# Performance work log

Hardware: AMD Instinct MI355X
Metric: run time of the kernel (lower is better)

## Reference

```python
import jax, jax.numpy as jnp
import numpy as np


def _lstm(x, Wk, Wr, b, reverse, return_seq):
    # Keras LSTM with activation='relu', recurrent_activation='sigmoid'.
    # Wk: (F, 4H), Wr: (H, 4H), b: (4H). Gate order: i, f, c, o.
    if reverse:
        x = jnp.flip(x, 1)
    H = Wr.shape[0]
    xg = jnp.einsum('btf,fg->btg', x, Wk) + b  # (B, T, 4H)
    B = x.shape[0]

    def step(carry, g_t):
        h, c = carry
        g = g_t + h @ Wr
        i = jax.nn.sigmoid(g[:, :H])
        f = jax.nn.sigmoid(g[:, H:2 * H])
        cc = jax.nn.relu(g[:, 2 * H:3 * H])
        o = jax.nn.sigmoid(g[:, 3 * H:])
        c = f * c + i * cc
        h = o * jax.nn.relu(c)
        return (h, c), h

    init = (jnp.zeros((B, H), x.dtype), jnp.zeros((B, H), x.dtype))
    (h, _), hs = jax.lax.scan(step, init, jnp.swapaxes(xg, 0, 1))
    if return_seq:
        hs = jnp.swapaxes(hs, 0, 1)  # (B, T, H)
        if reverse:
            hs = jnp.flip(hs, 1)
        return hs
    return h


def setup_inputs() -> dict:
    key = jax.random.key(0)
    ks = jax.random.split(key, 24)
    B, LA, T, F = 256, 200, 512, 128
    s = 0.05
    d = {
        'inputA': jax.random.randint(ks[0], (B, LA), 0, 1000),
        'inputB': jax.random.normal(ks[1], (B, T, F), jnp.float32),
        'emb': jax.random.normal(ks[2], (1000, 3), jnp.float32) * s,
        'w1': jax.random.normal(ks[3], (600, 256), jnp.float32) * s,
        'b1': jnp.zeros((256,), jnp.float32),
        'w2': jax.random.normal(ks[4], (256, 128), jnp.float32) * s,
        'b2': jnp.zeros((128,), jnp.float32),
        'w3': jax.random.normal(ks[5], (128, 64), jnp.float32) * s,
        'b3': jnp.zeros((64,), jnp.float32),
        'k1f': jax.random.normal(ks[6], (128, 512), jnp.float32) * s,
        'r1f': jax.random.normal(ks[7], (128, 512), jnp.float32) * s,
        'bb1f': jnp.zeros((512,), jnp.float32),
        'k1b': jax.random.normal(ks[8], (128, 512), jnp.float32) * s,
        'r1b': jax.random.normal(ks[9], (128, 512), jnp.float32) * s,
        'bb1b': jnp.zeros((512,), jnp.float32),
        'k2f': jax.random.normal(ks[10], (256, 256), jnp.float32) * s,
        'r2f': jax.random.normal(ks[11], (64, 256), jnp.float32) * s,
        'bb2f': jnp.zeros((256,), jnp.float32),
        'k2b': jax.random.normal(ks[12], (256, 256), jnp.float32) * s,
        'r2b': jax.random.normal(ks[13], (64, 256), jnp.float32) * s,
        'bb2b': jnp.zeros((256,), jnp.float32),
        'wz1': jax.random.normal(ks[14], (192, 2), jnp.float32) * s,
        'bz1': jnp.zeros((2,), jnp.float32),
        'wz2': jax.random.normal(ks[15], (2, 1), jnp.float32) * s,
        'bz2': jnp.zeros((1,), jnp.float32),
        'wt1': jax.random.normal(ks[16], (192, 2), jnp.float32) * s,
        'bt1': jnp.zeros((2,), jnp.float32),
        'wt2': jax.random.normal(ks[17], (2, 1), jnp.float32) * s,
        'bt2': jnp.zeros((1,), jnp.float32),
    }
    return d


def reference(inputA, inputB, emb, w1, b1, w2, b2, w3, b3,
              k1f, r1f, bb1f, k1b, r1b, bb1b,
              k2f, r2f, bb2f, k2b, r2b, bb2b,
              wz1, bz1, wz2, bz2, wt1, bt1, wt2, bt2):
    B = inputA.shape[0]
    # Embedding branch
    x = emb[inputA]                       # (B, LA, 3)
    x = x.reshape(B, -1)                  # flatten -> (B, 600)
    x = jax.nn.relu(x @ w1 + b1)
    x = jax.nn.relu(x @ w2 + b2)
    x = jax.nn.relu(x @ w3 + b3)          # (B, 64)
    # BiLSTM branch
    y_f = _lstm(inputB, k1f, r1f, bb1f, reverse=False, return_seq=True)
    y_b = _lstm(inputB, k1b, r1b, bb1b, reverse=True, return_seq=True)
    y = jnp.concatenate([y_f, y_b], axis=-1)   # (B, T, 256)
    h_f = _lstm(y, k2f, r2f, bb2f, reverse=False, return_seq=False)
    h_b = _lstm(y, k2b, r2b, bb2b, reverse=True, return_seq=False)
    y = jnp.concatenate([h_f, h_b], axis=-1)    # (B, 128)
    combined = jnp.concatenate([x, y], axis=-1)  # (B, 192)
    z = jax.nn.relu(combined @ wz1 + bz1) @ wz2 + bz2
    t = jax.nn.relu(combined @ wt1 + bt1) @ wt2 + bt2
    return (z, t)
```

## Files before the change

### kernel.cpp

```cpp
#include <hip/hip_runtime.h>

typedef __attribute__((ext_vector_type(8))) short s8v;
typedef __attribute__((ext_vector_type(4))) short s4v;
typedef __attribute__((ext_vector_type(4))) float f4v;

#if __has_builtin(__builtin_amdgcn_exp2f)
#define EXP2(x) __builtin_amdgcn_exp2f(x)
#else
#define EXP2(x) exp2f(x)
#endif
#if __has_builtin(__builtin_amdgcn_rcpf)
#define RCP(x) __builtin_amdgcn_rcpf(x)
#else
#define RCP(x) (1.0f/(x))
#endif

#define LOG2E 1.4426950408889634f

__device__ __forceinline__ short f2bf(float f) {
    union { float f; unsigned u; } x; x.f = f;
    unsigned r = (x.u + 0x7FFFu + ((x.u >> 16) & 1u)) >> 16;
    return (short)r;
}
__device__ __forceinline__ float bf2f(short s) {
    union { unsigned u; float f; } x; x.u = ((unsigned)(unsigned short)s) << 16;
    return x.f;
}
__device__ __forceinline__ void lds_barrier() {
    asm volatile("s_waitcnt lgkmcnt(0)\n\ts_barrier" ::: "memory");
}

__global__ __launch_bounds__(256) void prep_embed_kernel(
        const float* __restrict__ k1f, const float* __restrict__ r1f,
        const float* __restrict__ k1b, const float* __restrict__ r1b,
        const float* __restrict__ k2f, const float* __restrict__ r2f,
        const float* __restrict__ k2b, const float* __restrict__ r2b,
        short* __restrict__ WB1, short* __restrict__ WB2,
        const int* __restrict__ inputA, const float* __restrict__ emb,
        const float* __restrict__ w1, const float* __restrict__ b1,
        const float* __restrict__ w2, const float* __restrict__ b2,
        const float* __restrict__ w3, const float* __restrict__ b3,
        float* __restrict__ xe) {
    if (blockIdx.x < 1024) {
        int idx = blockIdx.x * 256 + threadIdx.x;
        if (idx < 262144) {
            int j = idx & 7, l = (idx >> 3) & 63, c = (idx >> 9) & 7, n = (idx >> 12) & 31, d = (idx >> 17) & 1;
            int coln = n * 16 + (l & 15);
            int k = c * 32 + ((l >> 4) * 8) + j;
            const float* Wk = d ? k1b : k1f;
            const float* Wr = d ? r1b : r1f;
            float v = (c < 4) ? Wk[k * 512 + coln] : Wr[(k - 128) * 512 + coln];
            float sc = ((n >> 3) == 2) ? 1.0f : -LOG2E;
            WB1[idx] = f2bf(v * sc);
        }
        if (idx < 163840) {
            int d = idx / 81920, r0 = idx % 81920;
            int n = r0 / 5120, r1 = r0 % 5120;
            int c = r1 / 512, li = r1 % 512;
            int l = li >> 3, j = li & 7;
            int coln = n * 16 + (l & 15);
            int k = c * 32 + ((l >> 4) * 8) + j;
            const float* Wk = d ? k2b : k2f;
            const float* Wr = d ? r2b : r2f;
            float v = (k < 256) ? Wk[k * 256 + coln] : Wr[(k - 256) * 256 + coln];
            float sc = ((n >> 2) == 2) ? 1.0f : -LOG2E;
            WB2[idx] = f2bf(v * sc);
        }
        return;
    }
    __shared__ float row[600];
    __shared__ float h1[256];
    __shared__ float h2[128];
    int b = blockIdx.x - 1024, t = threadIdx.x;
    if (t < 200) {
        int idx = inputA[b * 200 + t];
        row[t * 3 + 0] = emb[idx * 3 + 0];
        row[t * 3 + 1] = emb[idx * 3 + 1];
        row[t * 3 + 2] = emb[idx * 3 + 2];
    }
    __syncthreads();
    float a = b1[t];
    for (int k = 0; k < 600; k++) a += row[k] * w1[k * 256 + t];
    h1[t] = fmaxf(a, 0.f);
    __syncthreads();
    if (t < 128) {
        float a2 = b2[t];
        for (int k = 0; k < 256; k++) a2 += h1[k] * w2[k * 128 + t];
        h2[t] = fmaxf(a2, 0.f);
    }
    __syncthreads();
    if (t < 64) {
        float a3 = b3[t];
        for (int k = 0; k < 128; k++) a3 += h2[k] * w3[k * 64 + t];
        xe[b * 64 + t] = fmaxf(a3, 0.f);
    }
}

__global__ __launch_bounds__(512, 2) void megastep(
        const float* __restrict__ x, const short* __restrict__ WB1, const short* __restrict__ WB2,
        const float* __restrict__ bb1f, const float* __restrict__ bb1b,
        const float* __restrict__ bb2f, const float* __restrict__ bb2b,
        short* __restrict__ yfr, short* __restrict__ xgA, short* __restrict__ xgB,
        short* __restrict__ ygA, short* __restrict__ ygB,
        float* __restrict__ c1st, short* __restrict__ h1st,
        float* __restrict__ c2st, short* __restrict__ h2st,
        float* __restrict__ h2o, int k, int TC, int NC) {
    __shared__ short hA[2048];
    __shared__ short hB[2048];
    __shared__ short stg[38912];
    const int tid = threadIdx.x, lane = tid & 63, w = tid >> 6;
    const int bid = blockIdx.x;
    const int tgn = TC >> 3;

    if (bid < 32) {
        const int cl = k - 1;
        if (cl < 0 || cl >= NC) return;
        const int t0 = cl * TC;
        const int first = (cl == 0);
        const int btile = bid & 15, dir = bid >> 4;
        const int col = lane & 15, q = lane >> 4, u = (w << 4) + col;
        const int sb = dir * 16 + btile;

        s8v wf[4][4];
#pragma unroll
        for (int ti = 0; ti < 4; ti++)
#pragma unroll
            for (int c = 0; c < 4; c++)
                wf[ti][c] = *(const s8v*)(WB1 + ((((dir * 32 + (w + 8 * ti)) * 8) + 4 + c) * 64 + lane) * 8);

        float cst[4], hl[4];
        if (first) {
#pragma unroll
            for (int r = 0; r < 4; r++) cst[r] = 0.f;
            for (int i = tid; i < 2048; i += 512) hA[i] = 0;
        } else {
            f4v cv = *(const f4v*)(c1st + ((size_t)sb * 8 + w) * 256 + lane * 4);
#pragma unroll
            for (int r = 0; r < 4; r++) cst[r] = cv[r];
            for (int i = tid; i < 2048; i += 512) hA[i] = h1st[sb * 2048 + i];
        }
        __syncthreads();

        const short* xgp = ((cl & 1) ? xgB : xgA) + (size_t)sb * TC * 8192 + w * 1024 + lane * 8;
        s8v pe0 = *(const s8v*)(xgp);
        s8v pe1 = *(const s8v*)(xgp + 512);
        s8v po0 = *(const s8v*)(xgp + 8192);
        s8v po1 = *(const s8v*)(xgp + 8192 + 512);

        const int hidx = (w >> 1) * 512 + ((u >> 3) & 3) * 128 + (u & 7);

        for (int s = 0; s < TC; s += 2) {
            {
                s8v ah[4];
#pragma unroll
                for (int cc = 0; cc < 4; cc++) ah[cc] = *(const s8v*)&hA[(cc * 64 + lane) * 8];
                if (w >= 4 && s > 0) {
                    int tp = t0 + s - 1;
                    if (dir) tp = 511 - tp;
                    s8v hv = (w == 4) ? ah[0] : (w == 5) ? ah[1] : (w == 6) ? ah[2] : ah[3];
                    *(s8v*)(yfr + (((size_t)(btile * 512 + tp) * 8) + dir * 4 + (w - 4)) * 512 + lane * 8) = hv;
                }
                f4v acc[4];
#pragma unroll
                for (int r = 0; r < 4; r++) {
                    acc[0][r] = bf2f(pe0[r]);
                    acc[1][r] = bf2f(pe0[4 + r]);
                    acc[2][r] = bf2f(pe1[r]);
                    acc[3][r] = bf2f(pe1[4 + r]);
                }
                {
                    const short* np = xgp + (size_t)(s + 2) * 8192;
                    pe0 = *(const s8v*)np;
                    pe1 = *(const s8v*)(np + 512);
                }
#pragma unroll
                for (int cc = 0; cc < 4; cc++)
#pragma unroll
                    for (int ti = 0; ti < 4; ti++)
                        acc[ti] = __builtin_amdgcn_mfma_f32_16x16x32_bf16(ah[cc], wf[ti][cc], acc[ti], 0, 0, 0);
#pragma unroll
                for (int r = 0; r < 4; r++) {
                    float iv = RCP(1.0f + EXP2(acc[0][r]));
                    float fv = RCP(1.0f + EXP2(acc[1][r]));
                    float ov = RCP(1.0f + EXP2(acc[3][r]));
                    float ccv = fmaxf(acc[2][r], 0.f);
                    cst[r] = fv * cst[r] + iv * ccv;
                    hl[r] = ov * fmaxf(cst[r], 0.f);
                }
#pragma unroll
                for (int r = 0; r < 4; r++)
                    hB[hidx + ((q * 4 + r) << 3)] = f2bf(hl[r]);
                lds_barrier();
            }
            {
                s8v ah[4];
#pragma unroll
                for (int cc = 0; cc < 4; cc++) ah[cc] = *(const s8v*)&hB[(cc * 64 + lane) * 8];
                if (w >= 4) {
                    int tp = t0 + s;
                    if (dir) tp = 511 - tp;
                    s8v hv = (w == 4) ? ah[0] : (w == 5) ? ah[1] : (w == 6) ? ah[2] : ah[3];
                    *(s8v*)(yfr + (((size_t)(btile * 512 + tp) * 8) + dir * 4 + (w - 4)) * 512 + lane * 8) = hv;
                }
                f4v acc[4];
#pragma unroll
                for (int r = 0; r < 4; r++) {
                    acc[0][r] = bf2f(po0[r]);
                    acc[1][r] = bf2f(po0[4 + r]);
                    acc[2][r] = bf2f(po1[r]);
                    acc[3][r] = bf2f(po1[4 + r]);
                }
                {
                    const short* np = xgp + (size_t)(s + 3) * 8192;
                    po0 = *(const s8v*)np;
                    po1 = *(const s8v*)(np + 512);
                }
#pragma unroll
                for (int cc = 0; cc < 4; cc++)
#pragma unroll
                    for (int ti = 0; ti < 4; ti++)
                        acc[ti] = __builtin_amdgcn_mfma_f32_16x16x32_bf16(ah[cc], wf[ti][cc], acc[ti], 0, 0, 0);
#pragma unroll
                for (int r = 0; r < 4; r++) {
                    float iv = RCP(1.0f + EXP2(acc[0][r]));
                    float fv = RCP(1.0f + EXP2(acc[1][r]));
                    float ov = RCP(1.0f + EXP2(acc[3][r]));
                    float ccv = fmaxf(acc[2][r], 0.f);
                    cst[r] = fv * cst[r] + iv * ccv;
                    hl[r] = ov * fmaxf(cst[r], 0.f);
                }
#pragma unroll
                for (int r = 0; r < 4; r++)
                    hA[hidx + ((q * 4 + r) << 3)] = f2bf(hl[r]);
                lds_barrier();
            }
        }
        if (w >= 4) {
            int tp = t0 + TC - 1;
            if (dir) tp = 511 - tp;
            s8v hv = *(const s8v*)&hA[((w - 4) * 64 + lane) * 8];
            *(s8v*)(yfr + (((size_t)(btile * 512 + tp) * 8) + dir * 4 + (w - 4)) * 512 + lane * 8) = hv;
        }
        f4v cv;
#pragma unroll
        for (int r = 0; r < 4; r++) cv[r] = cst[r];
        *(f4v*)(c1st + ((size_t)sb * 8 + w) * 256 + lane * 4) = cv;
        for (int i = tid; i < 2048; i += 512) h1st[sb * 2048 + i] = hA[i];
        return;
    }

    if (bid < 64) {
        const int c2 = k - 3;
        if (c2 < 0 || c2 >= NC) return;
        const int first = (c2 == 0), last = (c2 == NC - 1);
        const int btile = (bid - 32) & 15, dir = (bid - 32) >> 4;
        const int b0 = btile << 4;
        const int w4 = w & 3;
        const int col = lane & 15, q = lane >> 4, u = (w4 << 4) + col;
        const int sb = dir * 16 + btile;

        s8v wf[4][2];
#pragma unroll
        for (int ti = 0; ti < 4; ti++)
#pragma unroll
            for (int c = 0; c < 2; c++)
                wf[ti][c] = *(const s8v*)(WB2 + ((((dir * 16 + (w4 + 4 * ti)) * 10) + 8 + c) * 64 + lane) * 8);

        float cst[4], hl[4] = {0.f, 0.f, 0.f, 0.f};
        if (first) {
#pragma unroll
            for (int r = 0; r < 4; r++) cst[r] = 0.f;
            for (int i = tid; i < 1024; i += 512) hA[i] = 0;
        } else {
            f4v cv = *(const f4v*)(c2st + ((size_t)sb * 4 + w4) * 256 + lane * 4);
#pragma unroll
            for (int r = 0; r < 4; r++) cst[r] = cv[r];
            for (int i = tid; i < 1024; i += 512) hA[i] = h2st[sb * 1024 + i];
        }
        __syncthreads();

        const short* ygp = ((c2 & 1) ? ygB : ygA) + (size_t)sb * TC * 4096 + w4 * 1024 + lane * 8;
        s8v pe0, pe1, po0, po1;
        if (w < 4) {
            pe0 = *(const s8v*)(ygp);
            pe1 = *(const s8v*)(ygp + 512);
            po0 = *(const s8v*)(ygp + 4096);
            po1 = *(const s8v*)(ygp + 4096 + 512);
        }
        const int hidx = (w4 >> 1) * 512 + ((u >> 3) & 3) * 128 + (u & 7);

        for (int s = 0; s < TC; s += 2) {
            if (w < 4) {
                s8v ah[2];
#pragma unroll
                for (int cc = 0; cc < 2; cc++) ah[cc] = *(const s8v*)&hA[(cc * 64 + lane) * 8];
                f4v acc[4];
#pragma unroll
                for (int r = 0; r < 4; r++) {
                    acc[0][r] = bf2f(pe0[r]);
                    acc[1][r] = bf2f(pe0[4 + r]);
                    acc[2][r] = bf2f(pe1[r]);
                    acc[3][r] = bf2f(pe1[4 + r]);
                }
                {
                    const short* np = ygp + (size_t)(s + 2) * 4096;
                    pe0 = *(const s8v*)np;
                    pe1 = *(const s8v*)(np + 512);
                }
#pragma unroll
                for (int cc = 0; cc < 2; cc++)
#pragma unroll
                    for (int ti = 0; ti < 4; ti++)
                        acc[ti] = __builtin_amdgcn_mfma_f32_16x16x32_bf16(ah[cc], wf[ti][cc], acc[ti], 0, 0, 0);
#pragma unroll
                for (int r = 0; r < 4; r++) {
                    float iv = RCP(1.0f + EXP2(acc[0][r]));
                    float fv = RCP(1.0f + EXP2(acc[1][r]));
                    float ov = RCP(1.0f + EXP2(acc[3][r]));
                    float ccv = fmaxf(acc[2][r], 0.f);
                    cst[r] = fv * cst[r] + iv * ccv;
                    hl[r] = ov * fmaxf(cst[r], 0.f);
                }
#pragma unroll
                for (int r = 0; r < 4; r++)
                    hB[hidx + ((q * 4 + r) << 3)] = f2bf(hl[r]);
            }
            lds_barrier();
            if (w < 4) {
                s8v ah[2];
#pragma unroll
                for (int cc = 0; cc < 2; cc++) ah[cc] = *(const s8v*)&hB[(cc * 64 + lane) * 8];
                f4v acc[4];
#pragma unroll
                for (int r = 0; r < 4; r++) {
                    acc[0][r] = bf2f(po0[r]);
                    acc[1][r] = bf2f(po0[4 + r]);
                    acc[2][r] = bf2f(po1[r]);
                    acc[3][r] = bf2f(po1[4 + r]);
                }
                {
                    const short* np = ygp + (size_t)(s + 3) * 4096;
                    po0 = *(const s8v*)np;
                    po1 = *(const s8v*)(np + 512);
                }
#pragma unroll
                for (int cc = 0; cc < 2; cc++)
#pragma unroll
                    for (int ti = 0; ti < 4; ti++)
                        acc[ti] = __builtin_amdgcn_mfma_f32_16x16x32_bf16(ah[cc], wf[ti][cc], acc[ti], 0, 0, 0);
#pragma unroll
                for (int r = 0; r < 4; r++) {
                    float iv = RCP(1.0f + EXP2(acc[0][r]));
                    float fv = RCP(1.0f + EXP2(acc[1][r]));
                    float ov = RCP(1.0f + EXP2(acc[3][r]));
                    float ccv = fmaxf(acc[2][r], 0.f);
                    cst[r] = fv * cst[r] + iv * ccv;
                    hl[r] = ov * fmaxf(cst[r], 0.f);
                }
#pragma unroll
                for (int r = 0; r < 4; r++)
                    hA[hidx + ((q * 4 + r) << 3)] = f2bf(hl[r]);
            }
            lds_barrier();
        }
        if (w < 4) {
            f4v cv;
#pragma unroll
            for (int r = 0; r < 4; r++) cv[r] = cst[r];
            *(f4v*)(c2st + ((size_t)sb * 4 + w4) * 256 + lane * 4) = cv;
        }
        __syncthreads();
        for (int i = tid; i < 1024; i += 512) h2st[sb * 1024 + i] = hA[i];
        if (last && w < 4) {
#pragma unroll
            for (int r = 0; r < 4; r++)
                h2o[((dir * 256) + b0 + q * 4 + r) * 64 + u] = hl[r];
        }
        return;
    }

    if (bid < 64 + 4 * TC) {
        const int cg = k;
        if (cg >= NC) return;
        const int t0 = cg * TC;
        const int g = bid - 64;
        const int btile = g & 15;
        const int rest = g >> 4;
        const int tg = rest % tgn;
        const int dir = rest / tgn;
        const int b0 = btile << 4;
        short* xg_w = (cg & 1) ? xgB : xgA;
        {
            int tglob = t0 + tg * 8 + w;
            if (dir) tglob = 511 - tglob;
            const int half = lane >> 5;
            const int f0 = (lane & 31) * 4;
            const int cx = f0 >> 5, qq = (f0 >> 3) & 3, j0 = f0 & 7;
#pragma unroll
            for (int rr = 0; rr < 8; rr++) {
                const int m = rr * 2 + half;
                const float* xp = x + ((size_t)(b0 + m) * 512 + tglob) * 128 + f0;
                f4v v4 = *(const f4v*)xp;
                const int slot = (qq << 4) | ((m ^ qq ^ (cx << 1)) & 15);
                s4v pk;
#pragma unroll
                for (int j = 0; j < 4; j++) pk[j] = f2bf(v4[j]);
                *(s4v*)&stg[(((w * 4 + cx) * 64 + slot) * 8) + j0] = pk;
            }
        }
        s8v wf[4][4];
#pragma unroll
        for (int ti = 0; ti < 4; ti++)
#pragma unroll
            for (int c = 0; c < 4; c++)
                wf[ti][c] = *(const s8v*)(WB1 + ((((dir * 32 + (w + 8 * ti)) * 8) + c) * 64 + lane) * 8);
        const float* bb = dir ? bb1b : bb1f;
        float bias[4];
#pragma unroll
        for (int ti = 0; ti < 4; ti++) {
            const int tile = w + 8 * ti;
            float sc = ((tile >> 3) == 2) ? 1.0f : -LOG2E;
            bias[ti] = sc * bb[tile * 16 + (lane & 15)];
        }
        __syncthreads();
        const size_t sb = dir * 16 + btile;
#pragma unroll 2
        for (int sl = 0; sl < 8; sl++) {
            s8v a[4];
#pragma unroll
            for (int c = 0; c < 4; c++) {
                const int slot = lane ^ (lane >> 4) ^ (c << 1);
                a[c] = *(const s8v*)&stg[((sl * 4 + c) * 64 + slot) * 8];
            }
            f4v acc[4];
#pragma unroll
            for (int ti = 0; ti < 4; ti++) { f4v z = {0.f, 0.f, 0.f, 0.f}; acc[ti] = z; }
#pragma unroll
            for (int c = 0; c < 4; c++)
#pragma unroll
                for (int ti = 0; ti < 4; ti++)
                    acc[ti] = __builtin_amdgcn_mfma_f32_16x16x32_bf16(a[c], wf[ti][c], acc[ti], 0, 0, 0);
            short* outp = xg_w + ((sb * TC + (size_t)(tg * 8 + sl)) * 8 + w) * 1024 + lane * 8;
#pragma unroll
            for (int p = 0; p < 2; p++) {
                s8v v;
#pragma unroll
                for (int j = 0; j < 4; j++) {
                    v[j]     = f2bf(acc[2 * p][j]     + bias[2 * p]);
                    v[4 + j] = f2bf(acc[2 * p + 1][j] + bias[2 * p + 1]);
                }
                *(s8v*)(outp + p * 512) = v;
            }
        }
        return;
    }

    {
        const int cg = k - 2;
        if (cg < 0 || cg >= NC) return;
        const int t0 = cg * TC;
        const int g = bid - 64 - 4 * TC;
        const int btile = g & 15;
        const int rest = g >> 4;
        const int tg = rest % tgn;
        const int dir = rest / tgn;
        short* yg_w = (cg & 1) ? ygB : ygA;
        const int w4 = w & 3, sh = (w >> 2) * 4;
        s8v wf[4][8];
#pragma unroll
        for (int ti = 0; ti < 4; ti++)
#pragma unroll
            for (int c = 0; c < 8; c++)
                wf[ti][c] = *(const s8v*)(WB2 + ((((dir * 16 + (w4 + 4 * ti)) * 10) + c) * 64 + lane) * 8);
        const float* bb = dir ? bb2b : bb2f;
        float bias[4];
#pragma unroll
        for (int ti = 0; ti < 4; ti++) {
            const int tile = w4 + 4 * ti;
            float sc = ((tile >> 2) == 2) ? 1.0f : -LOG2E;
            bias[ti] = sc * bb[tile * 16 + (lane & 15)];
        }
        const size_t sb = dir * 16 + btile;
#pragma unroll
        for (int si = 0; si < 4; si++) {
            const int sl = sh + si;
            int tglob = t0 + tg * 8 + sl;
            if (dir) tglob = 511 - tglob;
            s8v a[8];
#pragma unroll
            for (int c = 0; c < 8; c++)
                a[c] = *(const s8v*)(yfr + (((size_t)(btile * 512 + tglob) * 8) + c) * 512 + lane * 8);
            f4v acc[4];
#pragma unroll
            for (int ti = 0; ti < 4; ti++) { f4v z = {0.f, 0.f, 0.f, 0.f}; acc[ti] = z; }
#pragma unroll
            for (int c = 0; c < 8; c++)
#pragma unroll
                for (int ti = 0; ti < 4; ti++)
                    acc[ti] = __builtin_amdgcn_mfma_f32_16x16x32_bf16(a[c], wf[ti][c], acc[ti], 0, 0, 0);
            short* outp = yg_w + ((sb * TC + (size_t)(tg * 8 + sl)) * 4 + w4) * 1024 + lane * 8;
#pragma unroll
            for (int p = 0; p < 2; p++) {
                s8v v;
#pragma unroll
                for (int j = 0; j < 4; j++) {
                    v[j]     = f2bf(acc[2 * p][j]     + bias[2 * p]);
                    v[4 + j] = f2bf(acc[2 * p + 1][j] + bias[2 * p + 1]);
                }
                *(s8v*)(outp + p * 512) = v;
            }
        }
    }
}

__global__ void heads_kernel(const float* __restrict__ xe, const float* __restrict__ h2o,
                             const float* __restrict__ wz1, const float* __restrict__ bz1,
                             const float* __restrict__ wz2, const float* __restrict__ bz2,
                             const float* __restrict__ wt1, const float* __restrict__ bt1,
                             const float* __restrict__ wt2, const float* __restrict__ bt2,
                             float* __restrict__ out) {
    int b = threadIdx.x;
    float cz0 = bz1[0], cz1 = bz1[1], ct0 = bt1[0], ct1 = bt1[1];
    for (int k = 0; k < 192; k++) {
        float v = (k < 64) ? xe[b * 64 + k]
                : (k < 128) ? h2o[b * 64 + (k - 64)]
                            : h2o[(256 + b) * 64 + (k - 128)];
        cz0 += v * wz1[k * 2 + 0];
        cz1 += v * wz1[k * 2 + 1];
        ct0 += v * wt1[k * 2 + 0];
        ct1 += v * wt1[k * 2 + 1];
    }
    cz0 = fmaxf(cz0, 0.f); cz1 = fmaxf(cz1, 0.f);
    ct0 = fmaxf(ct0, 0.f); ct1 = fmaxf(ct1, 0.f);
    out[b] = cz0 * wz2[0] + cz1 * wz2[1] + bz2[0];
    out[256 + b] = ct0 * wt2[0] + ct1 * wt2[1] + bt2[0];
}

extern "C" void kernel_launch(void* const* d_in, const int* in_sizes, int n_in,
                              void* d_out, int out_size, void* d_ws, size_t ws_size,
                              hipStream_t stream) {
    const int*   inputA = (const int*)d_in[0];
    const float* inputB = (const float*)d_in[1];
    const float* emb = (const float*)d_in[2];
    const float* w1  = (const float*)d_in[3];
    const float* b1  = (const float*)d_in[4];
    const float* w2  = (const float*)d_in[5];
    const float* b2  = (const float*)d_in[6];
    const float* w3  = (const float*)d_in[7];
    const float* b3  = (const float*)d_in[8];
    const float* k1f = (const float*)d_in[9];
    const float* r1f = (const float*)d_in[10];
    const float* bb1f= (const float*)d_in[11];
    const float* k1b = (const float*)d_in[12];
    const float* r1b = (const float*)d_in[13];
    const float* bb1b= (const float*)d_in[14];
    const float* k2f = (const float*)d_in[15];
    const float* r2f = (const float*)d_in[16];
    const float* bb2f= (const float*)d_in[17];
    const float* k2b = (const float*)d_in[18];
    const float* r2b = (const float*)d_in[19];
    const float* bb2b= (const float*)d_in[20];
    const float* wz1 = (const float*)d_in[21];
    const float* bz1 = (const float*)d_in[22];
    const float* wz2 = (const float*)d_in[23];
    const float* bz2 = (const float*)d_in[24];
    const float* wt1 = (const float*)d_in[25];
    const float* bt1 = (const float*)d_in[26];
    const float* wt2 = (const float*)d_in[27];
    const float* bt2 = (const float*)d_in[28];

    char* ws = (char*)d_ws;
    short* WB1  = (short*)(ws);
    short* WB2  = (short*)(ws + 524288);
    float* xe   = (float*)(ws + 851968);
    float* h2o  = (float*)(ws + 917504);
    float* c1st = (float*)(ws + 1048576);
    short* h1st = (short*)(ws + 1310720);
    float* c2st = (float*)(ws + 1441792);
    short* h2st = (short*)(ws + 1572864);
    short* yfr  = (short*)(ws + 2097152);
    float* out  = (float*)d_out;

    int TC = 32;
    if (69206016ull + 2ull * 64 * 524288 + 2ull * 64 * 262144 + 65536 <= ws_size) TC = 64;
    const int NC = 512 / TC;
    short* xgA = (short*)(ws + 69206016);
    short* xgB = xgA + (size_t)TC * 262144;
    short* ygA = xgB + (size_t)TC * 262144;
    short* ygB = ygA + (size_t)TC * 131072;
    const int grid = 64 + 8 * TC;

    prep_embed_kernel<<<1280, 256, 0, stream>>>(k1f, r1f, k1b, r1b, k2f, r2f, k2b, r2b,
                                                WB1, WB2, inputA, emb, w1, b1, w2, b2, w3, b3, xe);
    for (int k = 0; k < NC + 3; k++) {
        megastep<<<grid, 512, 0, stream>>>(inputB, WB1, WB2, bb1f, bb1b, bb2f, bb2b,
                                           yfr, xgA, xgB, ygA, ygB,
                                           c1st, h1st, c2st, h2st, h2o, k, TC, NC);
    }
    heads_kernel<<<1, 256, 0, stream>>>(xe, h2o, wz1, bz1, wz2, bz2, wt1, bt1, wt2, bt2, out);
}
```

Measured before the change: 672.9 us.

## Deepen recurrent input prefetch to eight steps and cap grid at 256 blocks

The recurrent LSTM loops now prefetch the precomputed gate inputs eight timesteps ahead instead of two, using macro-expanded steps unrolled by eight. The goal is to hide global-load latency on the serial critical path. The projection work (layer-1 input GEMM and layer-2 input GEMM) is no longer given one block per task. It is distributed over a fixed 192 worker blocks in a grid-stride task loop, so the grid is fixed at 256 blocks and fits in one wave. This adds register pressure for the extra prefetch buffers and serialises some projection tasks per block. The TC=64 workspace threshold is also raised.

```diff
diff --git a/kernel.cpp b/kernel.cpp
--- a/kernel.cpp
+++ b/kernel.cpp
@@ -96,6 +96,77 @@
     }
 }
 
+#define L1_STEP(SRC, DST, PA, PB, SIDX) do { \
+    s8v ah[4]; \
+    _Pragma("unroll") \
+    for (int cc = 0; cc < 4; cc++) ah[cc] = *(const s8v*)&SRC[(cc * 64 + lane) * 8]; \
+    if (w >= 4 && (SIDX) > 0) { \
+        int tp = t0 + (SIDX) - 1; if (dir) tp = 511 - tp; \
+        s8v hv = (w == 4) ? ah[0] : (w == 5) ? ah[1] : (w == 6) ? ah[2] : ah[3]; \
+        *(s8v*)(ybase + (size_t)tp * 4096) = hv; \
+    } \
+    f4v acc[4]; \
+    _Pragma("unroll") \
+    for (int r = 0; r < 4; r++) { \
+        acc[0][r] = bf2f(PA[r]); acc[1][r] = bf2f(PA[4 + r]); \
+        acc[2][r] = bf2f(PB[r]); acc[3][r] = bf2f(PB[4 + r]); \
+    } \
+    { const short* np = xgp + (size_t)((SIDX) + 8) * 8192; \
+      PA = *(const s8v*)np; PB = *(const s8v*)(np + 512); } \
+    _Pragma("unroll") \
+    for (int cc = 0; cc < 4; cc++) { \
+        _Pragma("unroll") \
+        for (int ti = 0; ti < 4; ti++) \
+            acc[ti] = __builtin_amdgcn_mfma_f32_16x16x32_bf16(ah[cc], wf[ti][cc], acc[ti], 0, 0, 0); \
+    } \
+    _Pragma("unroll") \
+    for (int r = 0; r < 4; r++) { \
+        float iv = RCP(1.0f + EXP2(acc[0][r])); \
+        float fv = RCP(1.0f + EXP2(acc[1][r])); \
+        float ov = RCP(1.0f + EXP2(acc[3][r])); \
+        float ccv = fmaxf(acc[2][r], 0.f); \
+        cst[r] = fv * cst[r] + iv * ccv; \
+        hl[r] = ov * fmaxf(cst[r], 0.f); \
+    } \
+    _Pragma("unroll") \
+    for (int r = 0; r < 4; r++) DST[hidx + ((q * 4 + r) << 3)] = f2bf(hl[r]); \
+    lds_barrier(); \
+} while (0)
+
+#define L2_STEP(SRC, DST, PA, PB, SIDX) do { \
+    if (w < 4) { \
+        s8v ah[2]; \
+        _Pragma("unroll") \
+        for (int cc = 0; cc < 2; cc++) ah[cc] = *(const s8v*)&SRC[(cc * 64 + lane) * 8]; \
+        f4v acc[4]; \
+        _Pragma("unroll") \
+        for (int r = 0; r < 4; r++) { \
+            acc[0][r] = bf2f(PA[r]); acc[1][r] = bf2f(PA[4 + r]); \
+            acc[2][r] = bf2f(PB[r]); acc[3][r] = bf2f(PB[4 + r]); \
+        } \
+        { const short* np = ygp + (size_t)((SIDX) + 8) * 4096; \
+          PA = *(const s8v*)np; PB = *(const s8v*)(np + 512); } \
+        _Pragma("unroll") \
+        for (int cc = 0; cc < 2; cc++) { \
+            _Pragma("unroll") \
+            for (int ti = 0; ti < 4; ti++) \
+                acc[ti] = __builtin_amdgcn_mfma_f32_16x16x32_bf16(ah[cc], wf[ti][cc], acc[ti], 0, 0, 0); \
+        } \
+        _Pragma("unroll") \
+        for (int r = 0; r < 4; r++) { \
+            float iv = RCP(1.0f + EXP2(acc[0][r])); \
+            float fv = RCP(1.0f + EXP2(acc[1][r])); \
+            float ov = RCP(1.0f + EXP2(acc[3][r])); \
+            float ccv = fmaxf(acc[2][r], 0.f); \
+            cst[r] = fv * cst[r] + iv * ccv; \
+            hl[r] = ov * fmaxf(cst[r], 0.f); \
+        } \
+        _Pragma("unroll") \
+        for (int r = 0; r < 4; r++) DST[hidx + ((q * 4 + r) << 3)] = f2bf(hl[r]); \
+    } \
+    lds_barrier(); \
+} while (0)
+
 __global__ __launch_bounds__(512, 2) void megastep(
         const float* __restrict__ x, const short* __restrict__ WB1, const short* __restrict__ WB2,
         const float* __restrict__ bb1f, const float* __restrict__ bb1b,
@@ -142,104 +213,33 @@
         __syncthreads();
 
         const short* xgp = ((cl & 1) ? xgB : xgA) + (size_t)sb * TC * 8192 + w * 1024 + lane * 8;
-        s8v pe0 = *(const s8v*)(xgp);
-        s8v pe1 = *(const s8v*)(xgp + 512);
-        s8v po0 = *(const s8v*)(xgp + 8192);
-        s8v po1 = *(const s8v*)(xgp + 8192 + 512);
+        short* ybase = yfr + ((size_t)btile * 4096 + dir * 4 + ((w >= 4) ? (w - 4) : 0)) * 512 + lane * 8;
+        s8v E0a = *(const s8v*)(xgp + 0 * 8192), E0b = *(const s8v*)(xgp + 0 * 8192 + 512);
+        s8v O0a = *(const s8v*)(xgp + 1 * 8192), O0b = *(const s8v*)(xgp + 1 * 8192 + 512);
+        s8v E1a = *(const s8v*)(xgp + 2 * 8192), E1b = *(const s8v*)(xgp + 2 * 8192 + 512);
+        s8v O1a = *(const s8v*)(xgp + 3 * 8192), O1b = *(const s8v*)(xgp + 3 * 8192 + 512);
+        s8v E2a = *(const s8v*)(xgp + 4 * 8192), E2b = *(const s8v*)(xgp + 4 * 8192 + 512);
+        s8v O2a = *(const s8v*)(xgp + 5 * 8192), O2b = *(const s8v*)(xgp + 5 * 8192 + 512);
+        s8v E3a = *(const s8v*)(xgp + 6 * 8192), E3b = *(const s8v*)(xgp + 6 * 8192 + 512);
+        s8v O3a = *(const s8v*)(xgp + 7 * 8192), O3b = *(const s8v*)(xgp + 7 * 8192 + 512);
 
         const int hidx = (w >> 1) * 512 + ((u >> 3) & 3) * 128 + (u & 7);
 
-        for (int s = 0; s < TC; s += 2) {
-            {
-                s8v ah[4];
-#pragma unroll
-                for (int cc = 0; cc < 4; cc++) ah[cc] = *(const s8v*)&hA[(cc * 64 + lane) * 8];
-                if (w >= 4 && s > 0) {
-                    int tp = t0 + s - 1;
-                    if (dir) tp = 511 - tp;
-                    s8v hv = (w == 4) ? ah[0] : (w == 5) ? ah[1] : (w == 6) ? ah[2] : ah[3];
-                    *(s8v*)(yfr + (((size_t)(btile * 512 + tp) * 8) + dir * 4 + (w - 4)) * 512 + lane * 8) = hv;
-                }
-                f4v acc[4];
-#pragma unroll
-                for (int r = 0; r < 4; r++) {
-                    acc[0][r] = bf2f(pe0[r]);
-                    acc[1][r] = bf2f(pe0[4 + r]);
-                    acc[2][r] = bf2f(pe1[r]);
-                    acc[3][r] = bf2f(pe1[4 + r]);
-                }
-                {
-                    const short* np = xgp + (size_t)(s + 2) * 8192;
-                    pe0 = *(const s8v*)np;
-                    pe1 = *(const s8v*)(np + 512);
-                }
-#pragma unroll
-                for (int cc = 0; cc < 4; cc++)
-#pragma unroll
-                    for (int ti = 0; ti < 4; ti++)
-                        acc[ti] = __builtin_amdgcn_mfma_f32_16x16x32_bf16(ah[cc], wf[ti][cc], acc[ti], 0, 0, 0);
-#pragma unroll
-                for (int r = 0; r < 4; r++) {
-                    float iv = RCP(1.0f + EXP2(acc[0][r]));
-                    float fv = RCP(1.0f + EXP2(acc[1][r]));
-                    float ov = RCP(1.0f + EXP2(acc[3][r]));
-                    float ccv = fmaxf(acc[2][r], 0.f);
-                    cst[r] = fv * cst[r] + iv * ccv;
-                    hl[r] = ov * fmaxf(cst[r], 0.f);
-                }
-#pragma unroll
-                for (int r = 0; r < 4; r++)
-                    hB[hidx + ((q * 4 + r) << 3)] = f2bf(hl[r]);
-                lds_barrier();
-            }
-            {
-                s8v ah[4];
-#pragma unroll
-                for (int cc = 0; cc < 4; cc++) ah[cc] = *(const s8v*)&hB[(cc * 64 + lane) * 8];
-                if (w >= 4) {
-                    int tp = t0 + s;
-                    if (dir) tp = 511 - tp;
-                    s8v hv = (w == 4) ? ah[0] : (w == 5) ? ah[1] : (w == 6) ? ah[2] : ah[3];
-                    *(s8v*)(yfr + (((size_t)(btile * 512 + tp) * 8) + dir * 4 + (w - 4)) * 512 + lane * 8) = hv;
-                }
-                f4v acc[4];
-#pragma unroll
-                for (int r = 0; r < 4; r++) {
-                    acc[0][r] = bf2f(po0[r]);
-                    acc[1][r] = bf2f(po0[4 + r]);
-                    acc[2][r] = bf2f(po1[r]);
-                    acc[3][r] = bf2f(po1[4 + r]);
-                }
-                {
-                    const short* np = xgp + (size_t)(s + 3) * 8192;
-                    po0 = *(const s8v*)np;
-                    po1 = *(const s8v*)(np + 512);
-                }
-#pragma unroll
-                for (int cc = 0; cc < 4; cc++)
-#pragma unroll
-                    for (int ti = 0; ti < 4; ti++)
-                        acc[ti] = __builtin_amdgcn_mfma_f32_16x16x32_bf16(ah[cc], wf[ti][cc], acc[ti], 0, 0, 0);
-#pragma unroll
-                for (int r = 0; r < 4; r++) {
-                    float iv = RCP(1.0f + EXP2(acc[0][r]));
-                    float fv = RCP(1.0f + EXP2(acc[1][r]));
-                    float ov = RCP(1.0f + EXP2(acc[3][r]));
-                    float ccv = fmaxf(acc[2][r], 0.f);
-                    cst[r] = fv * cst[r] + iv * ccv;
-                    hl[r] = ov * fmaxf(cst[r], 0.f);
-                }
-#pragma unroll
-                for (int r = 0; r < 4; r++)
-                    hA[hidx + ((q * 4 + r) << 3)] = f2bf(hl[r]);
-                lds_barrier();
-            }
+        for (int s = 0; s < TC; s += 8) {
+            L1_STEP(hA, hB, E0a, E0b, s + 0);
+            L1_STEP(hB, hA, O0a, O0b, s + 1);
+            L1_STEP(hA, hB, E1a, E1b, s + 2);
+            L1_STEP(hB, hA, O1a, O1b, s + 3);
+            L1_STEP(hA, hB, E2a, E2b, s + 4);
+            L1_STEP(hB, hA, O2a, O2b, s + 5);
+            L1_STEP(hA, hB, E3a, E3b, s + 6);
+            L1_STEP(hB, hA, O3a, O3b, s + 7);
         }
         if (w >= 4) {
             int tp = t0 + TC - 1;
             if (dir) tp = 511 - tp;
             s8v hv = *(const s8v*)&hA[((w - 4) * 64 + lane) * 8];
-            *(s8v*)(yfr + (((size_t)(btile * 512 + tp) * 8) + dir * 4 + (w - 4)) * 512 + lane * 8) = hv;
+            *(s8v*)(ybase + (size_t)tp * 4096) = hv;
         }
         f4v cv;
 #pragma unroll
@@ -280,88 +280,28 @@
         __syncthreads();
 
         const short* ygp = ((c2 & 1) ? ygB : ygA) + (size_t)sb * TC * 4096 + w4 * 1024 + lane * 8;
-        s8v pe0, pe1, po0, po1;
+        s8v E0a, E0b, O0a, O0b, E1a, E1b, O1a, O1b, E2a, E2b, O2a, O2b, E3a, E3b, O3a, O3b;
         if (w < 4) {
-            pe0 = *(const s8v*)(ygp);
-            pe1 = *(const s8v*)(ygp + 512);
-            po0 = *(const s8v*)(ygp + 4096);
-            po1 = *(const s8v*)(ygp + 4096 + 512);
+            E0a = *(const s8v*)(ygp + 0 * 4096); E0b = *(const s8v*)(ygp + 0 * 4096 + 512);
+            O0a = *(const s8v*)(ygp + 1 * 4096); O0b = *(const s8v*)(ygp + 1 * 4096 + 512);
+            E1a = *(const s8v*)(ygp + 2 * 4096); E1b = *(const s8v*)(ygp + 2 * 4096 + 512);
+            O1a = *(const s8v*)(ygp + 3 * 4096); O1b = *(const s8v*)(ygp + 3 * 4096 + 512);
+            E2a = *(const s8v*)(ygp + 4 * 4096); E2b = *(const s8v*)(ygp + 4 * 4096 + 512);
+            O2a = *(const s8v*)(ygp + 5 * 4096); O2b = *(const s8v*)(ygp + 5 * 4096 + 512);
+            E3a = *(const s8v*)(ygp + 6 * 4096); E3b = *(const s8v*)(ygp + 6 * 4096 + 512);
+            O3a = *(const s8v*)(ygp + 7 * 4096); O3b = *(const s8v*)(ygp + 7 * 4096 + 512);
         }
         const int hidx = (w4 >> 1) * 512 + ((u >> 3) & 3) * 128 + (u & 7);
 
-        for (int s = 0; s < TC; s += 2) {
-            if (w < 4) {
-                s8v ah[2];
-#pragma unroll
-                for (int cc = 0; cc < 2; cc++) ah[cc] = *(const s8v*)&hA[(cc * 64 + lane) * 8];
-                f4v acc[4];
-#pragma unroll
-                for (int r = 0; r < 4; r++) {
-                    acc[0][r] = bf2f(pe0[r]);
-                    acc[1][r] = bf2f(pe0[4 + r]);
-                    acc[2][r] = bf2f(pe1[r]);
-                    acc[3][r] = bf2f(pe1[4 + r]);
-                }
-                {
-                    const short* np = ygp + (size_t)(s + 2) * 4096;
-                    pe0 = *(const s8v*)np;
-                    pe1 = *(const s8v*)(np + 512);
-                }
-#pragma unroll
-                for (int cc = 0; cc < 2; cc++)
-#pragma unroll
-                    for (int ti = 0; ti < 4; ti++)
-                        acc[ti] = __builtin_amdgcn_mfma_f32_16x16x32_bf16(ah[cc], wf[ti][cc], acc[ti], 0, 0, 0);
-#pragma unroll
-                for (int r = 0; r < 4; r++) {
-                    float iv = RCP(1.0f + EXP2(acc[0][r]));
-                    float fv = RCP(1.0f + EXP2(acc[1][r]));
-                    float ov = RCP(1.0f + EXP2(acc[3][r]));
-                    float ccv = fmaxf(acc[2][r], 0.f);
-                    cst[r] = fv * cst[r] + iv * ccv;
-                    hl[r] = ov * fmaxf(cst[r], 0.f);
-                }
-#pragma unroll
-                for (int r = 0; r < 4; r++)
-                    hB[hidx + ((q * 4 + r) << 3)] = f2bf(hl[r]);
-            }
-            lds_barrier();
-            if (w < 4) {
-                s8v ah[2];
-#pragma unroll
-                for (int cc = 0; cc < 2; cc++) ah[cc] = *(const s8v*)&hB[(cc * 64 + lane) * 8];
-                f4v acc[4];
-#pragma unroll
-                for (int r = 0; r < 4; r++) {
-                    acc[0][r] = bf2f(po0[r]);
-                    acc[1][r] = bf2f(po0[4 + r]);
-                    acc[2][r] = bf2f(po1[r]);
-                    acc[3][r] = bf2f(po1[4 + r]);
-                }
-                {
-                    const short* np = ygp + (size_t)(s + 3) * 4096;
-                    po0 = *(const s8v*)np;
-                    po1 = *(const s8v*)(np + 512);
-                }
-#pragma unroll
-                for (int cc = 0; cc < 2; cc++)
-#pragma unroll
-                    for (int ti = 0; ti < 4; ti++)
-                        acc[ti] = __builtin_amdgcn_mfma_f32_16x16x32_bf16(ah[cc], wf[ti][cc], acc[ti], 0, 0, 0);
-#pragma unroll
-                for (int r = 0; r < 4; r++) {
-                    float iv = RCP(1.0f + EXP2(acc[0][r]));
-                    float fv = RCP(1.0f + EXP2(acc[1][r]));
-                    float ov = RCP(1.0f + EXP2(acc[3][r]));
-                    float ccv = fmaxf(acc[2][r], 0.f);
-                    cst[r] = fv * cst[r] + iv * ccv;
-                    hl[r] = ov * fmaxf(cst[r], 0.f);
-                }
-#pragma unroll
-                for (int r = 0; r < 4; r++)
-                    hA[hidx + ((q * 4 + r) << 3)] = f2bf(hl[r]);
-            }
-            lds_barrier();
+        for (int s = 0; s < TC; s += 8) {
+            L2_STEP(hA, hB, E0a, E0b, s + 0);
+            L2_STEP(hB, hA, O0a, O0b, s + 1);
+            L2_STEP(hA, hB, E1a, E1b, s + 2);
+            L2_STEP(hB, hA, O1a, O1b, s + 3);
+            L2_STEP(hA, hB, E2a, E2b, s + 4);
+            L2_STEP(hB, hA, O2a, O2b, s + 5);
+            L2_STEP(hA, hB, E3a, E3b, s + 6);
+            L2_STEP(hB, hA, O3a, O3b, s + 7);
         }
         if (w < 4) {
             f4v cv;
@@ -379,135 +319,138 @@
         return;
     }
 
-    if (bid < 64 + 4 * TC) {
-        const int cg = k;
-        if (cg >= NC) return;
-        const int t0 = cg * TC;
-        const int g = bid - 64;
-        const int btile = g & 15;
-        const int rest = g >> 4;
-        const int tg = rest % tgn;
-        const int dir = rest / tgn;
-        const int b0 = btile << 4;
-        short* xg_w = (cg & 1) ? xgB : xgA;
-        {
-            int tglob = t0 + tg * 8 + w;
-            if (dir) tglob = 511 - tglob;
-            const int half = lane >> 5;
-            const int f0 = (lane & 31) * 4;
-            const int cx = f0 >> 5, qq = (f0 >> 3) & 3, j0 = f0 & 7;
-#pragma unroll
-            for (int rr = 0; rr < 8; rr++) {
-                const int m = rr * 2 + half;
-                const float* xp = x + ((size_t)(b0 + m) * 512 + tglob) * 128 + f0;
-                f4v v4 = *(const f4v*)xp;
-                const int slot = (qq << 4) | ((m ^ qq ^ (cx << 1)) & 15);
-                s4v pk;
-#pragma unroll
-                for (int j = 0; j < 4; j++) pk[j] = f2bf(v4[j]);
-                *(s4v*)&stg[(((w * 4 + cx) * 64 + slot) * 8) + j0] = pk;
-            }
-        }
-        s8v wf[4][4];
-#pragma unroll
-        for (int ti = 0; ti < 4; ti++)
-#pragma unroll
-            for (int c = 0; c < 4; c++)
-                wf[ti][c] = *(const s8v*)(WB1 + ((((dir * 32 + (w + 8 * ti)) * 8) + c) * 64 + lane) * 8);
-        const float* bb = dir ? bb1b : bb1f;
-        float bias[4];
-#pragma unroll
-        for (int ti = 0; ti < 4; ti++) {
-            const int tile = w + 8 * ti;
-            float sc = ((tile >> 3) == 2) ? 1.0f : -LOG2E;
-            bias[ti] = sc * bb[tile * 16 + (lane & 15)];
-        }
-        __syncthreads();
-        const size_t sb = dir * 16 + btile;
+    {
+        const int wid = bid - 64;
+        const int n1 = (k < NC) ? 4 * TC : 0;
+        const int n2 = (k >= 2 && (k - 2) < NC) ? 4 * TC : 0;
+        for (int tsk = wid; tsk < n1 + n2; tsk += 192) {
+            if (tsk < n1) {
+                const int cg = k;
+                const int t0 = cg * TC;
+                const int g = tsk;
+                const int btile = g & 15;
+                const int rest = g >> 4;
+                const int tg = rest % tgn;
+                const int dir = rest / tgn;
+                const int b0 = btile << 4;
+                short* xg_w = (cg & 1) ? xgB : xgA;
+                __syncthreads();
+                {
+                    int tglob = t0 + tg * 8 + w;
+                    if (dir) tglob = 511 - tglob;
+                    const int half = lane >> 5;
+                    const int f0 = (lane & 31) * 4;
+                    const int cx = f0 >> 5, qq = (f0 >> 3) & 3, j0 = f0 & 7;
+#pragma unroll
+                    for (int rr = 0; rr < 8; rr++) {
+                        const int m = rr * 2 + half;
+                        const float* xp = x + ((size_t)(b0 + m) * 512 + tglob) * 128 + f0;
+                        f4v v4 = *(const f4v*)xp;
+                        const int slot = (qq << 4) | ((m ^ qq ^ (cx << 1)) & 15);
+                        s4v pk;
+#pragma unroll
+                        for (int j = 0; j < 4; j++) pk[j] = f2bf(v4[j]);
+                        *(s4v*)&stg[(((w * 4 + cx) * 64 + slot) * 8) + j0] = pk;
+                    }
+                }
+                s8v wf[4][4];
+#pragma unroll
+                for (int ti = 0; ti < 4; ti++)
+#pragma unroll
+                    for (int c = 0; c < 4; c++)
+                        wf[ti][c] = *(const s8v*)(WB1 + ((((dir * 32 + (w + 8 * ti)) * 8) + c) * 64 + lane) * 8);
+                const float* bb = dir ? bb1b : bb1f;
+                float bias[4];
+#pragma unroll
+                for (int ti = 0; ti < 4; ti++) {
+                    const int tile = w + 8 * ti;
+                    float sc = ((tile >> 3) == 2) ? 1.0f : -LOG2E;
+                    bias[ti] = sc * bb[tile * 16 + (lane & 15)];
+                }
+                __syncthreads();
+                const size_t sb = dir * 16 + btile;
 #pragma unroll 2
-        for (int sl = 0; sl < 8; sl++) {
-            s8v a[4];
-#pragma unroll
-            for (int c = 0; c < 4; c++) {
-                const int slot = lane ^ (lane >> 4) ^ (c << 1);
-                a[c] = *(const s8v*)&stg[((sl * 4 + c) * 64 + slot) * 8];
-            }
-            f4v acc[4];
-#pragma unroll
-            for (int ti = 0; ti < 4; ti++) { f4v z = {0.f, 0.f, 0.f, 0.f}; acc[ti] = z; }
-#pragma unroll
-            for (int c = 0; c < 4; c++)
+                for (int sl = 0; sl < 8; sl++) {
+                    s8v a[4];
+#pragma unroll
+                    for (int c = 0; c < 4; c++) {
+                        const int slot = lane ^ (lane >> 4) ^ (c << 1);
+                        a[c] = *(const s8v*)&stg[((sl * 4 + c) * 64 + slot) * 8];
+                    }
+                    f4v acc[4];
+#pragma unroll
+                    for (int ti = 0; ti < 4; ti++) { f4v z = {0.f, 0.f, 0.f, 0.f}; acc[ti] = z; }
+#pragma unroll
+                    for (int c = 0; c < 4; c++)
+#pragma unroll
+                        for (int ti = 0; ti < 4; ti++)
+                            acc[ti] = __builtin_amdgcn_mfma_f32_16x16x32_bf16(a[c], wf[ti][c], acc[ti], 0, 0, 0);
+                    short* outp = xg_w + ((sb * TC + (size_t)(tg * 8 + sl)) * 8 + w) * 1024 + lane * 8;
+#pragma unroll
+                    for (int p = 0; p < 2; p++) {
+                        s8v v;
+#pragma unroll
+                        for (int j = 0; j < 4; j++) {
+                            v[j]     = f2bf(acc[2 * p][j]     + bias[2 * p]);
+                            v[4 + j] = f2bf(acc[2 * p + 1][j] + bias[2 * p + 1]);
+                        }
+                        *(s8v*)(outp + p * 512) = v;
+                    }
+                }
+            } else {
+                const int cg = k - 2;
+                const int t0 = cg * TC;
+                const int g = tsk - n1;
+                const int btile = g & 15;
+                const int rest = g >> 4;
+                const int tg = rest % tgn;
+                const int dir = rest / tgn;
+                short* yg_w = (cg & 1) ? ygB : ygA;
+                const int w4 = w & 3, sh = (w >> 2) * 4;
+                s8v wf[4][8];
 #pragma unroll
                 for (int ti = 0; ti < 4; ti++)
-                    acc[ti] = __builtin_amdgcn_mfma_f32_16x16x32_bf16(a[c], wf[ti][c], acc[ti], 0, 0, 0);
-            short* outp = xg_w + ((sb * TC + (size_t)(tg * 8 + sl)) * 8 + w) * 1024 + lane * 8;
-#pragma unroll
-            for (int p = 0; p < 2; p++) {
-                s8v v;
-#pragma unroll
-                for (int j = 0; j < 4; j++) {
-                    v[j]     = f2bf(acc[2 * p][j]     + bias[2 * p]);
-                    v[4 + j] = f2bf(acc[2 * p + 1][j] + bias[2 * p + 1]);
+#pragma unroll
+                    for (int c = 0; c < 8; c++)
+                        wf[ti][c] = *(const s8v*)(WB2 + ((((dir * 16 + (w4 + 4 * ti)) * 10) + c) * 64 + lane) * 8);
+                const float* bb = dir ? bb2b : bb2f;
+                float bias[4];
+#pragma unroll
+                for (int ti = 0; ti < 4; ti++) {
+                    const int tile = w4 + 4 * ti;
+                    float sc = ((tile >> 2) == 2) ? 1.0f : -LOG2E;
+                    bias[ti] = sc * bb[tile * 16 + (lane & 15)];
                 }
-                *(s8v*)(outp + p * 512) = v;
-            }
-        }
-        return;
-    }
-
-    {
-        const int cg = k - 2;
-        if (cg < 0 || cg >= NC) return;
-        const int t0 = cg * TC;
-        const int g = bid - 64 - 4 * TC;
-        const int btile = g & 15;
-        const int rest = g >> 4;
-        const int tg = rest % tgn;
-        const int dir = rest / tgn;
-        short* yg_w = (cg & 1) ? ygB : ygA;
-        const int w4 = w & 3, sh = (w >> 2) * 4;
-        s8v wf[4][8];
-#pragma unroll
-        for (int ti = 0; ti < 4; ti++)
-#pragma unroll
-            for (int c = 0; c < 8; c++)
-                wf[ti][c] = *(const s8v*)(WB2 + ((((dir * 16 + (w4 + 4 * ti)) * 10) + c) * 64 + lane) * 8);
-        const float* bb = dir ? bb2b : bb2f;
-        float bias[4];
-#pragma unroll
-        for (int ti = 0; ti < 4; ti++) {
-            const int tile = w4 + 4 * ti;
-            float sc = ((tile >> 2) == 2) ? 1.0f : -LOG2E;
-            bias[ti] = sc * bb[tile * 16 + (lane & 15)];
-        }
-        const size_t sb = dir * 16 + btile;
-#pragma unroll
-        for (int si = 0; si < 4; si++) {
-            const int sl = sh + si;
-            int tglob = t0 + tg * 8 + sl;
-            if (dir) tglob = 511 - tglob;
-            s8v a[8];
-#pragma unroll
-            for (int c = 0; c < 8; c++)
-                a[c] = *(const s8v*)(yfr + (((size_t)(btile * 512 + tglob) * 8) + c) * 512 + lane * 8);
-            f4v acc[4];
-#pragma unroll
-            for (int ti = 0; ti < 4; ti++) { f4v z = {0.f, 0.f, 0.f, 0.f}; acc[ti] = z; }
-#pragma unroll
-            for (int c = 0; c < 8; c++)
-#pragma unroll
-                for (int ti = 0; ti < 4; ti++)
-                    acc[ti] = __builtin_amdgcn_mfma_f32_16x16x32_bf16(a[c], wf[ti][c], acc[ti], 0, 0, 0);
-            short* outp = yg_w + ((sb * TC + (size_t)(tg * 8 + sl)) * 4 + w4) * 1024 + lane * 8;
-#pragma unroll
-            for (int p = 0; p < 2; p++) {
-                s8v v;
-#pragma unroll
-                for (int j = 0; j < 4; j++) {
-                    v[j]     = f2bf(acc[2 * p][j]     + bias[2 * p]);
-                    v[4 + j] = f2bf(acc[2 * p + 1][j] + bias[2 * p + 1]);
+                const size_t sb = dir * 16 + btile;
+#pragma unroll
+                for (int si = 0; si < 4; si++) {
+                    const int sl = sh + si;
+                    int tglob = t0 + tg * 8 + sl;
+                    if (dir) tglob = 511 - tglob;
+                    s8v a[8];
+#pragma unroll
+                    for (int c = 0; c < 8; c++)
+                        a[c] = *(const s8v*)(yfr + (((size_t)(btile * 512 + tglob) * 8) + c) * 512 + lane * 8);
+                    f4v acc[4];
+#pragma unroll
+                    for (int ti = 0; ti < 4; ti++) { f4v z = {0.f, 0.f, 0.f, 0.f}; acc[ti] = z; }
+#pragma unroll
+                    for (int c = 0; c < 8; c++)
+#pragma unroll
+                        for (int ti = 0; ti < 4; ti++)
+                            acc[ti] = __builtin_amdgcn_mfma_f32_16x16x32_bf16(a[c], wf[ti][c], acc[ti], 0, 0, 0);
+                    short* outp = yg_w + ((sb * TC + (size_t)(tg * 8 + sl)) * 4 + w4) * 1024 + lane * 8;
+#pragma unroll
+                    for (int p = 0; p < 2; p++) {
+                        s8v v;
+#pragma unroll
+                        for (int j = 0; j < 4; j++) {
+                            v[j]     = f2bf(acc[2 * p][j]     + bias[2 * p]);
+                            v[4 + j] = f2bf(acc[2 * p + 1][j] + bias[2 * p + 1]);
+                        }
+                        *(s8v*)(outp + p * 512) = v;
+                    }
                 }
-                *(s8v*)(outp + p * 512) = v;
             }
         }
     }
@@ -582,13 +525,13 @@
     float* out  = (float*)d_out;
 
     int TC = 32;
-    if (69206016ull + 2ull * 64 * 524288 + 2ull * 64 * 262144 + 65536 <= ws_size) TC = 64;
+    if (69206016ull + 2ull * 64 * 524288 + 2ull * 64 * 262144 + 262144 <= ws_size) TC = 64;
     const int NC = 512 / TC;
     short* xgA = (short*)(ws + 69206016);
     short* xgB = xgA + (size_t)TC * 262144;
     short* ygA = xgB + (size_t)TC * 262144;
     short* ygB = ygA + (size_t)TC * 131072;
-    const int grid = 64 + 8 * TC;
+    const int grid = 256;
 
     prep_embed_kernel<<<1280, 256, 0, stream>>>(k1f, r1f, k1b, r1b, k2f, r2f, k2b, r2b,
                                                 WB1, WB2, inputA, emb, w1, b1, w2, b2, w3, b3, xe);
```

Result: no change. 681.3 us (+1.3%).
